# Kernel tuning notes

Measured on AMD Instinct MI355X. Metric: run time of the kernel, lower is better.

Reference implementation:

```python
import jax, jax.numpy as jnp
import numpy as np

G, N, F_IN, H, C = 128, 512, 128, 128, 10
LAMB = 1.0
NEG_SLOPE = 0.2
P_EDGE = 32.0 / N  # avg degree ~32


def setup_inputs() -> dict:
    key = jax.random.key(0)
    ks = jax.random.split(key, 12)
    x = jax.random.normal(ks[0], (G, N, F_IN), dtype=jnp.float32)
    # symmetric 0/1 adjacency without self loops (per-graph dense block)
    a = (jax.random.uniform(ks[1], (G, N, N)) < P_EDGE).astype(jnp.float32)
    adj = jnp.maximum(a, jnp.swapaxes(a, 1, 2)) * (1.0 - jnp.eye(N, dtype=jnp.float32))

    def lin(k, fi, fo):
        return (jax.random.normal(k, (fi, fo), dtype=jnp.float32) / np.float32(np.sqrt(fi)))

    return {
        "x": x, "adj": adj,
        "W1": lin(ks[2], F_IN, H), "b1": jnp.zeros((H,), jnp.float32),
        "W2": lin(ks[3], H, H), "b2": jnp.zeros((H,), jnp.float32),
        "W3": lin(ks[4], H, H), "b3": jnp.zeros((H,), jnp.float32),
        "att1_s": 0.1 * jax.random.normal(ks[5], (H,), dtype=jnp.float32),
        "att1_d": 0.1 * jax.random.normal(ks[6], (H,), dtype=jnp.float32),
        "att2_s": 0.1 * jax.random.normal(ks[7], (H,), dtype=jnp.float32),
        "att2_d": 0.1 * jax.random.normal(ks[8], (H,), dtype=jnp.float32),
        "Wl1": lin(ks[9], 2 * H, H), "bl1": jnp.zeros((H,), jnp.float32),
        "Wl2": lin(ks[10], H, H // 2), "bl2": jnp.zeros((H // 2,), jnp.float32),
        "Wl3": lin(ks[11], H // 2, C), "bl3": jnp.zeros((C,), jnp.float32),
    }


def gcn(x, adj, W, b):
    # GCNConv: D^{-1/2} (A + I) D^{-1/2} X W + b  (self-loop weight 1, edge weights in adj)
    deg = adj.sum(-1) + 1.0                              # [G, n]
    dinv = jax.lax.rsqrt(deg)
    xw = x @ W                                           # [G, n, H]
    agg = jnp.einsum('gij,gjf->gif', adj, dinv[..., None] * xw)
    return dinv[..., None] * agg + (dinv * dinv)[..., None] * xw + b


def info_score(x, adj):
    # HGP-SL node information score: row-wise L1 norm of (I - D^{-1} A) X
    deg = jnp.maximum(adj.sum(-1), 1.0)
    agg = jnp.einsum('gij,gjf->gif', adj, x) / deg[..., None]
    return jnp.sum(jnp.abs(x - agg), axis=-1)            # [G, n]


def hgpsl_pool(x, adj, att_s, att_d, k):
    # top-k node selection by information score, then structure learning:
    # dense (sample=False) path: e_ij = leaky_relu(att.[x_i||x_j]) + lamb*A_ij, softmax over j
    s = info_score(x, adj)
    _, idx = jax.lax.top_k(s, k)                         # [G, k]
    xk = jnp.take_along_axis(x, idx[..., None], axis=1)  # [G, k, H]
    g = jnp.arange(x.shape[0])[:, None, None]
    ak = adj[g, idx[:, :, None], idx[:, None, :]]        # induced adjacency [G, k, k]
    e = jax.nn.leaky_relu((xk @ att_s)[:, :, None] + (xk @ att_d)[:, None, :], NEG_SLOPE)
    attn = jax.nn.softmax(e + LAMB * ak, axis=-1)        # new learned edge weights
    return xk, attn


def readout(x):
    # gmp || gap over nodes
    return jnp.concatenate([x.max(axis=1), x.mean(axis=1)], axis=-1)


def reference(x, adj, W1, b1, W2, b2, W3, b3, att1_s, att1_d, att2_s, att2_d,
              Wl1, bl1, Wl2, bl2, Wl3, bl3):
    h = jax.nn.relu(gcn(x, adj, W1, b1))
    h, a1 = hgpsl_pool(h, adj, att1_s, att1_d, N // 2)
    x1 = readout(h)
    h = jax.nn.relu(gcn(h, a1, W2, b2))
    h, a2 = hgpsl_pool(h, a1, att2_s, att2_d, N // 4)
    x2 = readout(h)
    h = jax.nn.relu(gcn(h, a2, W3, b3))
    x3 = readout(h)
    z = jax.nn.relu(x1) + jax.nn.relu(x2) + jax.nn.relu(x3)
    z = jax.nn.relu(z @ Wl1 + bl1)
    z = jax.nn.relu(z @ Wl2 + bl2)
    return jax.nn.softmax(z @ Wl3 + bl3, axis=-1)
```

## Files before the change

### kernel.cpp

```cpp
#include <hip/hip_runtime.h>

#define Gg   128
#define N1   512
#define FH   128
#define K1   256
#define K2   128

typedef __bf16 bf16x8 __attribute__((ext_vector_type(8)));
typedef float  floatx4 __attribute__((ext_vector_type(4)));

__device__ inline float wredsum(float v) {
#pragma unroll
    for (int o = 32; o; o >>= 1) v += __shfl_xor(v, o, 64);
    return v;
}
__device__ inline float wredmax(float v) {
#pragma unroll
    for (int o = 32; o; o >>= 1) v = fmaxf(v, __shfl_xor(v, o, 64));
    return v;
}
__device__ inline unsigned short bf_rne(float x) {
    unsigned u = __float_as_uint(x);
    return (unsigned short)((u + 0x7fffu + ((u >> 16) & 1u)) >> 16);
}

__global__ __launch_bounds__(256) void k_prep(const float* __restrict__ adj,
        float* __restrict__ dinv_gcn, float* __restrict__ dinv_info) {
    int wave = threadIdx.x >> 6, lane = threadIdx.x & 63;
    long long row = (long long)blockIdx.x * 4 + wave;
    const float* ar = adj + row * N1;
    float s = 0.f;
#pragma unroll
    for (int c = 0; c < 2; ++c) {
        float4 v = *(const float4*)(ar + lane * 8 + c * 4);
        s += (v.x + v.y) + (v.z + v.w);
    }
    s = wredsum(s);
    if (lane == 0) {
        dinv_gcn[row]  = rsqrtf(s + 1.0f);
        dinv_info[row] = 1.0f / fmaxf(s, 1.0f);
    }
}

__global__ __launch_bounds__(256) void k_tsplit(const float* __restrict__ feat,
        unsigned short* __restrict__ Thi, unsigned short* __restrict__ Tmid,
        unsigned short* __restrict__ Tlo) {
    __shared__ float tile[64 * 65];
    int b = blockIdx.x;
    int g = b >> 4, rb = (b >> 1) & 7, cb = b & 1;
    int t = threadIdx.x;
    {
        int r0 = t >> 4, c4 = t & 15;
#pragma unroll
        for (int i = 0; i < 4; ++i) {
            int r = r0 + i * 16;
            float4 v = *(const float4*)(feat + ((long long)g * 512 + rb * 64 + r) * 128 + cb * 64 + c4 * 4);
            tile[r * 65 + c4 * 4 + 0] = v.x;
            tile[r * 65 + c4 * 4 + 1] = v.y;
            tile[r * 65 + c4 * 4 + 2] = v.z;
            tile[r * 65 + c4 * 4 + 3] = v.w;
        }
    }
    __syncthreads();
    int tf = t >> 2, chunk = t & 3;
    unsigned short hbuf[16] __attribute__((aligned(16)));
    unsigned short mbuf[16] __attribute__((aligned(16)));
    unsigned short lbuf[16] __attribute__((aligned(16)));
#pragma unroll
    for (int i = 0; i < 16; ++i) {
        int m = chunk * 16 + i;
        float v = tile[m * 65 + tf];
        unsigned short h = bf_rne(v);
        float fh = __uint_as_float((unsigned)h << 16);
        float r1 = v - fh;
        unsigned short md = bf_rne(r1);
        float fm = __uint_as_float((unsigned)md << 16);
        float r2 = r1 - fm;
        unsigned short lo = bf_rne(r2);
        hbuf[i] = h; mbuf[i] = md; lbuf[i] = lo;
    }
    long long obase = ((long long)g * 128 + cb * 64 + tf) * 512 + rb * 64 + chunk * 16;
    *(uint4*)(Thi + obase)      = *(const uint4*)&hbuf[0];
    *(uint4*)(Thi + obase + 8)  = *(const uint4*)&hbuf[8];
    *(uint4*)(Tmid + obase)     = *(const uint4*)&mbuf[0];
    *(uint4*)(Tmid + obase + 8) = *(const uint4*)&mbuf[8];
    *(uint4*)(Tlo + obase)      = *(const uint4*)&lbuf[0];
    *(uint4*)(Tlo + obase + 8)  = *(const uint4*)&lbuf[8];
}

template<int EPI>
__global__ __launch_bounds__(256) void k_aggmm(const float* __restrict__ adjf,
        const unsigned short* __restrict__ Bhi, const unsigned short* __restrict__ Bmid,
        const unsigned short* __restrict__ Blo,
        const float* __restrict__ dvec, const float* __restrict__ hx,
        const float* __restrict__ bias, float* __restrict__ outH, float* __restrict__ outS) {
    __shared__ unsigned short Al[128 * 40];
    __shared__ unsigned short Bls[3][128 * 40];
    __shared__ float sred[2][128];
    int b = blockIdx.x;
    int g  = (b & 7) + ((b >> 5) << 3);
    int rb = (b >> 3) & 3;
    int tid = threadIdx.x;
    int w = tid >> 6, lane = tid & 63;
    int wm = w >> 1, wn = w & 1;
    int ln = lane & 15, quad = lane >> 4;
    floatx4 acc[4][4];
#pragma unroll
    for (int i = 0; i < 4; ++i)
#pragma unroll
        for (int j = 0; j < 4; ++j) { floatx4 z = {0.f, 0.f, 0.f, 0.f}; acc[i][j] = z; }

    const long long arow0 = ((long long)g * 512 + rb * 128) * 512;
    for (int kk = 0; kk < 512; kk += 32) {
        __syncthreads();
#pragma unroll
        for (int i = 0; i < 4; ++i) {
            int id = tid + i * 256;
            int r = id >> 3, c = id & 7;
            float4 v = *(const float4*)(adjf + arow0 + (long long)r * 512 + kk + c * 4);
            ushort4 u;
            u.x = (unsigned short)(__float_as_uint(v.x) >> 16);
            u.y = (unsigned short)(__float_as_uint(v.y) >> 16);
            u.z = (unsigned short)(__float_as_uint(v.z) >> 16);
            u.w = (unsigned short)(__float_as_uint(v.w) >> 16);
            *(ushort4*)&Al[r * 40 + c * 4] = u;
        }
#pragma unroll
        for (int mB = 0; mB < 3; ++mB) {
            const unsigned short* Bp = (mB == 0) ? Bhi : (mB == 1 ? Bmid : Blo);
#pragma unroll
            for (int i = 0; i < 2; ++i) {
                int id = tid + i * 256;
                int r = id >> 2, c = id & 3;
                uint4 u = *(const uint4*)(Bp + ((long long)g * 128 + r) * 512 + kk + c * 8);
                *(uint4*)&Bls[mB][r * 40 + c * 8] = u;
            }
        }
        __syncthreads();
        bf16x8 af[4];
#pragma unroll
        for (int tm = 0; tm < 4; ++tm)
            af[tm] = *(const bf16x8*)&Al[(wm * 64 + tm * 16 + ln) * 40 + quad * 8];
#pragma unroll
        for (int s = 0; s < 3; ++s) {
#pragma unroll
            for (int tn = 0; tn < 4; ++tn) {
                bf16x8 bfr = *(const bf16x8*)&Bls[s][(wn * 64 + tn * 16 + ln) * 40 + quad * 8];
#pragma unroll
                for (int tm = 0; tm < 4; ++tm)
                    acc[tm][tn] = __builtin_amdgcn_mfma_f32_16x16x32_bf16(af[tm], bfr, acc[tm][tn], 0, 0, 0);
            }
        }
    }
    long long rowbase = (long long)g * 512 + rb * 128;
    if (EPI == 0) {
#pragma unroll
        for (int tm = 0; tm < 4; ++tm)
#pragma unroll
        for (int r = 0; r < 4; ++r) {
            int ml = wm * 64 + tm * 16 + quad * 4 + r;
            long long grow = rowbase + ml;
            float di = dvec[grow];
#pragma unroll
            for (int tn = 0; tn < 4; ++tn) {
                int nc = wn * 64 + tn * 16 + ln;
                float hv = hx[grow * 128 + nc];
                float o = fmaxf(fmaf(di, acc[tm][tn][r] + hv, bias[nc]), 0.f);
                outH[grow * 128 + nc] = o;
            }
        }
    } else {
#pragma unroll
        for (int tm = 0; tm < 4; ++tm)
#pragma unroll
        for (int r = 0; r < 4; ++r) {
            int ml = wm * 64 + tm * 16 + quad * 4 + r;
            long long grow = rowbase + ml;
            float di = dvec[grow];
            float v = 0.f;
#pragma unroll
            for (int tn = 0; tn < 4; ++tn) {
                int nc = wn * 64 + tn * 16 + ln;
                float hv = hx[grow * 128 + nc];
                v += fabsf(hv - acc[tm][tn][r] * di);
            }
            v += __shfl_xor(v, 1); v += __shfl_xor(v, 2);
            v += __shfl_xor(v, 4); v += __shfl_xor(v, 8);
            if (ln == 0) sred[wn][ml] = v;
        }
        __syncthreads();
        if (tid < 128) outS[rowbase + tid] = sred[0][tid] + sred[1][tid];
    }
}

__global__ __launch_bounds__(256) void k_gemm_rw(const float* __restrict__ A,
        const float* __restrict__ W, float* __restrict__ C,
        const float* __restrict__ rs) {
    __shared__ float Al[64][68];
    __shared__ float Wl[64][132];
    long long row0 = (long long)blockIdx.x * 64;
    int tid = threadIdx.x, tr = tid >> 4, tc = tid & 15;
    float acc[4][8] = {};
    for (int ch = 0; ch < 2; ++ch) {
        for (int p = tid; p < 1024; p += 256) {
            int r = p >> 4, c4 = p & 15;
            *(float4*)&Al[r][c4 * 4] = *(const float4*)(A + (row0 + r) * 128 + ch * 64 + c4 * 4);
        }
        for (int p = tid; p < 2048; p += 256) {
            int r = p >> 5, c4 = p & 31;
            *(float4*)&Wl[r][c4 * 4] = *(const float4*)(W + (ch * 64 + r) * 128 + c4 * 4);
        }
        __syncthreads();
        for (int k = 0; k < 64; ++k) {
            float4 w0 = *(const float4*)&Wl[k][tc * 8];
            float4 w1 = *(const float4*)&Wl[k][tc * 8 + 4];
            float w[8] = {w0.x, w0.y, w0.z, w0.w, w1.x, w1.y, w1.z, w1.w};
#pragma unroll
            for (int i = 0; i < 4; ++i) {
                float a = Al[tr * 4 + i][k];
#pragma unroll
                for (int j = 0; j < 8; ++j) acc[i][j] = fmaf(a, w[j], acc[i][j]);
            }
        }
        __syncthreads();
    }
#pragma unroll
    for (int i = 0; i < 4; ++i) {
        long long r = row0 + tr * 4 + i;
        float sc = rs ? rs[r] : 1.0f;
        *(float4*)(C + r * 128 + tc * 8)     = make_float4(sc * acc[i][0], sc * acc[i][1], sc * acc[i][2], sc * acc[i][3]);
        *(float4*)(C + r * 128 + tc * 8 + 4) = make_float4(sc * acc[i][4], sc * acc[i][5], sc * acc[i][6], sc * acc[i][7]);
    }
}

template<int NT, int KSEL>
__global__ __launch_bounds__(256) void k_topk(const float* __restrict__ s, int* __restrict__ idx) {
    __shared__ unsigned long long keys[NT];
    int g = blockIdx.x;
    const float* sg = s + g * NT;
    for (int t = threadIdx.x; t < NT; t += 256) {
        unsigned int b = __float_as_uint(sg[t]);
        unsigned int ord = (b & 0x80000000u) ? ~b : (b | 0x80000000u);
        keys[t] = ((unsigned long long)(~ord) << 32) | (unsigned int)t;
    }
    __syncthreads();
    for (int k = 2; k <= NT; k <<= 1) {
        for (int j = k >> 1; j > 0; j >>= 1) {
            for (int i = threadIdx.x; i < NT; i += 256) {
                int l = i ^ j;
                if (l > i) {
                    bool dir = ((i & k) == 0);
                    unsigned long long a = keys[i], b2 = keys[l];
                    bool sw = dir ? (a > b2) : (a < b2);
                    if (sw) { keys[i] = b2; keys[l] = a; }
                }
            }
            __syncthreads();
        }
    }
    for (int t = threadIdx.x; t < KSEL; t += 256)
        idx[g * KSEL + t] = (int)(keys[t] & 0xffffffffu);
}

template<int KK>
__global__ __launch_bounds__(256) void k_gather(const float* __restrict__ h, int srcN,
        const int* __restrict__ idx, const float* __restrict__ atts, const float* __restrict__ attd,
        float* __restrict__ xk, float* __restrict__ as_, float* __restrict__ ad_) {
    int wave = threadIdx.x >> 6, lane = threadIdx.x & 63;
    int r = blockIdx.x * 4 + wave;
    int g = r / KK;
    int j = idx[r];
    float2 v = *(const float2*)(h + ((long long)g * srcN + j) * 128 + lane * 2);
    *(float2*)(xk + (long long)r * 128 + lane * 2) = v;
    float2 sv = *(const float2*)(atts + lane * 2);
    float2 dv = *(const float2*)(attd + lane * 2);
    float ps = v.x * sv.x + v.y * sv.y;
    float pd = v.x * dv.x + v.y * dv.y;
    ps = wredsum(ps); pd = wredsum(pd);
    if (lane == 0) { as_[r] = ps; ad_[r] = pd; }
}

template<int KK, int SRCN>
__global__ __launch_bounds__(256) void k_attn(const float* __restrict__ adjSrc,
        const int* __restrict__ idx, const float* __restrict__ as_, const float* __restrict__ ad_,
        float* __restrict__ attn, float* __restrict__ dgo, float* __restrict__ dio) {
    constexpr int E = KK / 64;
    __shared__ int   idxL[KK];
    __shared__ float adL[KK];
    __shared__ float rowL[4][SRCN];
    int bpg = KK / 4;
    int g = blockIdx.x / bpg;
    int wave = threadIdx.x >> 6, lane = threadIdx.x & 63;
    int i = (blockIdx.x % bpg) * 4 + wave;
    for (int t = threadIdx.x; t < KK; t += 256) { idxL[t] = idx[g * KK + t]; adL[t] = ad_[g * KK + t]; }
    __syncthreads();
    int ri = idxL[i];
    const float* arow = adjSrc + ((long long)g * SRCN + ri) * SRCN;
    for (int c = lane; c < SRCN; c += 64) rowL[wave][c] = arow[c];
    float asi = as_[g * KK + i];
    float vals[E];
    float m = -1e30f;
#pragma unroll
    for (int e = 0; e < E; ++e) {
        int j = e * 64 + lane;
        float x = asi + adL[j];
        x = (x >= 0.f) ? x : 0.2f * x;
        x += rowL[wave][idxL[j]];
        vals[e] = x; m = fmaxf(m, x);
    }
    m = wredmax(m);
    float S = 0.f;
#pragma unroll
    for (int e = 0; e < E; ++e) { vals[e] = expf(vals[e] - m); S += vals[e]; }
    S = wredsum(S);
    float inv = 1.f / S, rs = 0.f;
    float* orow = attn + ((long long)g * KK + i) * KK;
#pragma unroll
    for (int e = 0; e < E; ++e) { float p = vals[e] * inv; rs += p; orow[e * 64 + lane] = p; }
    rs = wredsum(rs);
    if (lane == 0) { dgo[g * KK + i] = rsqrtf(rs + 1.f); dio[g * KK + i] = 1.f / fmaxf(rs, 1.f); }
}

template<int KK>
__global__ __launch_bounds__(128) void k_readout(const float* __restrict__ xk, float* __restrict__ xo) {
    int g = blockIdx.x, f = threadIdx.x;
    const float* p = xk + (long long)g * KK * 128 + f;
    float m = -1e30f, s = 0.f;
    for (int r = 0; r < KK; ++r) { float v = p[r * 128]; m = fmaxf(m, v); s += v; }
    xo[g * 256 + f] = m;
    xo[g * 256 + 128 + f] = s * (1.0f / KK);
}

template<int KK, bool SCALEY, int EPI>
__global__ __launch_bounds__(256) void k_agg(const float* __restrict__ A, const float* __restrict__ Y,
        const float* __restrict__ dg, const float* __restrict__ di_,
        const float* __restrict__ bias, const float* __restrict__ hx,
        float* __restrict__ outH, float* __restrict__ outS) {
    __shared__ float Al[64][68];
    __shared__ float Yl[64][132];
    __shared__ float red[64][17];
    constexpr int RB = KK / 64;
    int g = blockIdx.x / RB;
    int rb = blockIdx.x % RB;
    const float* Ag = A + (long long)g * KK * KK;
    const float* Yg = Y + (long long)g * KK * 128;
    int tid = threadIdx.x, tr = tid >> 4, tc = tid & 15;
    float acc[4][8] = {};
    for (int ch = 0; ch < KK / 64; ++ch) {
        for (int p = tid; p < 1024; p += 256) {
            int r = p >> 4, c4 = p & 15;
            *(float4*)&Al[r][c4 * 4] = *(const float4*)(Ag + (rb * 64 + r) * KK + ch * 64 + c4 * 4);
        }
        for (int p = tid; p < 2048; p += 256) {
            int r = p >> 5, c4 = p & 31;
            float4 v = *(const float4*)(Yg + (ch * 64 + r) * 128 + c4 * 4);
            if (SCALEY) { float sc = dg[g * KK + ch * 64 + r]; v.x *= sc; v.y *= sc; v.z *= sc; v.w *= sc; }
            *(float4*)&Yl[r][c4 * 4] = v;
        }
        __syncthreads();
        for (int k = 0; k < 64; ++k) {
            float4 w0 = *(const float4*)&Yl[k][tc * 8];
            float4 w1 = *(const float4*)&Yl[k][tc * 8 + 4];
            float w[8] = {w0.x, w0.y, w0.z, w0.w, w1.x, w1.y, w1.z, w1.w};
#pragma unroll
            for (int i = 0; i < 4; ++i) {
                float a = Al[tr * 4 + i][k];
#pragma unroll
                for (int j = 0; j < 8; ++j) acc[i][j] = fmaf(a, w[j], acc[i][j]);
            }
        }
        __syncthreads();
    }
    int i0 = rb * 64 + tr * 4;
    if (EPI == 0) {
#pragma unroll
        for (int i = 0; i < 4; ++i) {
            long long gi = (long long)g * KK + i0 + i;
            float d = dg[gi], dd = d * d;
            float4 x0 = *(const float4*)(hx + gi * 128 + tc * 8);
            float4 x1 = *(const float4*)(hx + gi * 128 + tc * 8 + 4);
            float4 b0 = *(const float4*)(bias + tc * 8);
            float4 b1 = *(const float4*)(bias + tc * 8 + 4);
            float4 o0, o1;
            o0.x = fmaxf(fmaf(d, acc[i][0], fmaf(dd, x0.x, b0.x)), 0.f);
            o0.y = fmaxf(fmaf(d, acc[i][1], fmaf(dd, x0.y, b0.y)), 0.f);
            o0.z = fmaxf(fmaf(d, acc[i][2], fmaf(dd, x0.z, b0.z)), 0.f);
            o0.w = fmaxf(fmaf(d, acc[i][3], fmaf(dd, x0.w, b0.w)), 0.f);
            o1.x = fmaxf(fmaf(d, acc[i][4], fmaf(dd, x1.x, b1.x)), 0.f);
            o1.y = fmaxf(fmaf(d, acc[i][5], fmaf(dd, x1.y, b1.y)), 0.f);
            o1.z = fmaxf(fmaf(d, acc[i][6], fmaf(dd, x1.z, b1.z)), 0.f);
            o1.w = fmaxf(fmaf(d, acc[i][7], fmaf(dd, x1.w, b1.w)), 0.f);
            *(float4*)(outH + gi * 128 + tc * 8)     = o0;
            *(float4*)(outH + gi * 128 + tc * 8 + 4) = o1;
        }
    } else {
#pragma unroll
        for (int i = 0; i < 4; ++i) {
            long long gi = (long long)g * KK + i0 + i;
            float d = di_[gi];
            float4 x0 = *(const float4*)(hx + gi * 128 + tc * 8);
            float4 x1 = *(const float4*)(hx + gi * 128 + tc * 8 + 4);
            float p = fabsf(x0.x - acc[i][0] * d) + fabsf(x0.y - acc[i][1] * d)
                    + fabsf(x0.z - acc[i][2] * d) + fabsf(x0.w - acc[i][3] * d)
                    + fabsf(x1.x - acc[i][4] * d) + fabsf(x1.y - acc[i][5] * d)
                    + fabsf(x1.z - acc[i][6] * d) + fabsf(x1.w - acc[i][7] * d);
            red[tr * 4 + i][tc] = p;
        }
        __syncthreads();
        if (tid < 64) {
            float s = 0.f;
#pragma unroll
            for (int t = 0; t < 16; ++t) s += red[tid][t];
            outS[(long long)g * KK + rb * 64 + tid] = s;
        }
    }
}

__global__ __launch_bounds__(128) void k_mlp(const float* __restrict__ x1, const float* __restrict__ x2,
        const float* __restrict__ x3,
        const float* __restrict__ Wl1, const float* __restrict__ bl1,
        const float* __restrict__ Wl2, const float* __restrict__ bl2,
        const float* __restrict__ Wl3, const float* __restrict__ bl3,
        float* __restrict__ out) {
    __shared__ float z[256], z1[128], z2[64], lg[10];
    int g = blockIdx.x, t = threadIdx.x;
    for (int k = t; k < 256; k += 128)
        z[k] = fmaxf(x1[g * 256 + k], 0.f) + fmaxf(x2[g * 256 + k], 0.f) + fmaxf(x3[g * 256 + k], 0.f);
    __syncthreads();
    {
        float acc = bl1[t];
        for (int k = 0; k < 256; ++k) acc = fmaf(z[k], Wl1[k * 128 + t], acc);
        z1[t] = fmaxf(acc, 0.f);
    }
    __syncthreads();
    if (t < 64) {
        float acc = bl2[t];
        for (int k = 0; k < 128; ++k) acc = fmaf(z1[k], Wl2[k * 64 + t], acc);
        z2[t] = fmaxf(acc, 0.f);
    }
    __syncthreads();
    if (t < 10) {
        float acc = bl3[t];
        for (int k = 0; k < 64; ++k) acc = fmaf(z2[k], Wl3[k * 10 + t], acc);
        lg[t] = acc;
    }
    __syncthreads();
    if (t == 0) {
        float m = -1e30f;
        for (int c = 0; c < 10; ++c) m = fmaxf(m, lg[c]);
        float S = 0.f;
        float e[10];
        for (int c = 0; c < 10; ++c) { e[c] = expf(lg[c] - m); S += e[c]; }
        float inv = 1.f / S;
        for (int c = 0; c < 10; ++c) out[g * 10 + c] = e[c] * inv;
    }
}

extern "C" void kernel_launch(void* const* d_in, const int* in_sizes, int n_in,
                              void* d_out, int out_size, void* d_ws, size_t ws_size,
                              hipStream_t stream) {
    const float* x     = (const float*)d_in[0];
    const float* adj   = (const float*)d_in[1];
    const float* W1    = (const float*)d_in[2];
    const float* b1    = (const float*)d_in[3];
    const float* W2    = (const float*)d_in[4];
    const float* b2    = (const float*)d_in[5];
    const float* W3    = (const float*)d_in[6];
    const float* b3    = (const float*)d_in[7];
    const float* att1s = (const float*)d_in[8];
    const float* att1d = (const float*)d_in[9];
    const float* att2s = (const float*)d_in[10];
    const float* att2d = (const float*)d_in[11];
    const float* Wl1   = (const float*)d_in[12];
    const float* bl1   = (const float*)d_in[13];
    const float* Wl2   = (const float*)d_in[14];
    const float* bl2   = (const float*)d_in[15];
    const float* Wl3   = (const float*)d_in[16];
    const float* bl3   = (const float*)d_in[17];
    float* out = (float*)d_out;

    char* ws = (char*)d_ws;
    unsigned short* Thi  = (unsigned short*)(ws + 0);
    unsigned short* Tmid = (unsigned short*)(ws + 16777216);
    unsigned short* Tlo  = (unsigned short*)(ws + 33554432);
    float* xk1 = (float*)(ws + 0);
    float* xw2 = (float*)(ws + 16777216);
    float* h2  = (float*)(ws + 33554432);
    float* xk2 = (float*)(ws + 16777216);
    float* a2  = (float*)(ws + 25165824);
    float* xw3 = (float*)(ws + 0);
    float* h3  = (float*)(ws + 8388608);
    float* dxw1 = (float*)(ws + 50331648);
    float* h1   = dxw1;
    float* a1   = dxw1;
    float* s1      = (float*)(ws + 83886080);
    int*   idx1    = (int*)  (ws + 84148224);
    float* as1     = (float*)(ws + 84279296);
    float* ad1     = (float*)(ws + 84410368);
    float* dinv_g1 = (float*)(ws + 84541440);
    float* dinv_i1 = (float*)(ws + 84803584);
    float* dinv_g2 = (float*)(ws + 85065728);
    float* dinv_i2 = (float*)(ws + 85196800);
    float* x1r     = (float*)(ws + 85327872);
    float* s2      = (float*)(ws + 85458944);
    int*   idx2    = (int*)  (ws + 85590016);
    float* as2     = (float*)(ws + 85655552);
    float* ad2     = (float*)(ws + 85721088);
    float* dinv_g3 = (float*)(ws + 85786624);
    float* dinv_i3 = (float*)(ws + 85852160);
    float* x2r     = (float*)(ws + 85917696);
    float* x3r     = (float*)(ws + 86048768);

    k_prep<<<Gg * N1 / 4, 256, 0, stream>>>(adj, dinv_g1, dinv_i1);
    k_gemm_rw<<<Gg * N1 / 64, 256, 0, stream>>>(x, W1, dxw1, dinv_g1);
    k_tsplit<<<Gg * 16, 256, 0, stream>>>(dxw1, Thi, Tmid, Tlo);
    k_aggmm<0><<<Gg * 4, 256, 0, stream>>>(adj, Thi, Tmid, Tlo, dinv_g1, dxw1, b1, h1, nullptr);
    k_tsplit<<<Gg * 16, 256, 0, stream>>>(h1, Thi, Tmid, Tlo);
    k_aggmm<1><<<Gg * 4, 256, 0, stream>>>(adj, Thi, Tmid, Tlo, dinv_i1, h1, nullptr, nullptr, s1);
    k_topk<N1, K1><<<Gg, 256, 0, stream>>>(s1, idx1);
    k_gather<K1><<<Gg * K1 / 4, 256, 0, stream>>>(h1, N1, idx1, att1s, att1d, xk1, as1, ad1);
    k_readout<K1><<<Gg, 128, 0, stream>>>(xk1, x1r);
    k_attn<K1, N1><<<Gg * K1 / 4, 256, 0, stream>>>(adj, idx1, as1, ad1, a1, dinv_g2, dinv_i2);

    k_gemm_rw<<<Gg * K1 / 64, 256, 0, stream>>>(xk1, W2, xw2, nullptr);
    k_agg<K1, true, 0><<<Gg * (K1 / 64), 256, 0, stream>>>(a1, xw2, dinv_g2, dinv_i2, b2, xw2, h2, nullptr);
    k_agg<K1, false, 1><<<Gg * (K1 / 64), 256, 0, stream>>>(a1, h2, dinv_g2, dinv_i2, b2, h2, nullptr, s2);
    k_topk<K1, K2><<<Gg, 256, 0, stream>>>(s2, idx2);
    k_gather<K2><<<Gg * K2 / 4, 256, 0, stream>>>(h2, K1, idx2, att2s, att2d, xk2, as2, ad2);
    k_readout<K2><<<Gg, 128, 0, stream>>>(xk2, x2r);
    k_attn<K2, K1><<<Gg * K2 / 4, 256, 0, stream>>>(a1, idx2, as2, ad2, a2, dinv_g3, dinv_i3);

    k_gemm_rw<<<Gg * K2 / 64, 256, 0, stream>>>(xk2, W3, xw3, nullptr);
    k_agg<K2, true, 0><<<Gg * (K2 / 64), 256, 0, stream>>>(a2, xw3, dinv_g3, dinv_i3, b3, xw3, h3, nullptr);
    k_readout<K2><<<Gg, 128, 0, stream>>>(h3, x3r);

    k_mlp<<<Gg, 128, 0, stream>>>(x1r, x2r, x3r, Wl1, bl1, Wl2, bl2, Wl3, bl3, out);
}
```

Baseline: 606.8 us.

## Fuse bf16 splitting into GEMM epilogues and use MFMA for pooled-graph aggregation

The transpose-and-split kernels are removed. The three-way bf16 split is now written directly from the feature GEMM and GCN aggregation epilogues, and k_prep writes a bf16 copy of the adjacency so the aggregation loads half the bytes. The later pooled-level aggregations, which previously used scalar fp32 k_agg, now run on MFMA with 3-way split attention matrices produced by new attn kernels. In exchange the workspace grows a lot, and there is extra split work plus several shared-memory passes in the epilogues.

```diff
diff --git a/kernel.cpp b/kernel.cpp
--- a/kernel.cpp
+++ b/kernel.cpp
@@ -6,6 +6,7 @@
 #define K1   256
 #define K2   128
 
+typedef unsigned short ush;
 typedef __bf16 bf16x8 __attribute__((ext_vector_type(8)));
 typedef float  floatx4 __attribute__((ext_vector_type(4)));
 
@@ -19,22 +20,37 @@
     for (int o = 32; o; o >>= 1) v = fmaxf(v, __shfl_xor(v, o, 64));
     return v;
 }
-__device__ inline unsigned short bf_rne(float x) {
+__device__ inline ush bf_rne(float x) {
     unsigned u = __float_as_uint(x);
-    return (unsigned short)((u + 0x7fffu + ((u >> 16) & 1u)) >> 16);
+    return (ush)((u + 0x7fffu + ((u >> 16) & 1u)) >> 16);
+}
+__device__ inline float bf2f(ush u) { return __uint_as_float((unsigned)u << 16); }
+__device__ inline void split3(float v, ush& h, ush& m, ush& l) {
+    h = bf_rne(v);
+    float r1 = v - bf2f(h);
+    m = bf_rne(r1);
+    l = bf_rne(r1 - bf2f(m));
 }
 
 __global__ __launch_bounds__(256) void k_prep(const float* __restrict__ adj,
-        float* __restrict__ dinv_gcn, float* __restrict__ dinv_info) {
+        float* __restrict__ dinv_gcn, float* __restrict__ dinv_info,
+        ush* __restrict__ adjbf) {
     int wave = threadIdx.x >> 6, lane = threadIdx.x & 63;
     long long row = (long long)blockIdx.x * 4 + wave;
     const float* ar = adj + row * N1;
+    ush* br = adjbf + row * N1;
     float s = 0.f;
+    ush ub[8] __attribute__((aligned(16)));
 #pragma unroll
     for (int c = 0; c < 2; ++c) {
         float4 v = *(const float4*)(ar + lane * 8 + c * 4);
         s += (v.x + v.y) + (v.z + v.w);
-    }
+        ub[c * 4 + 0] = (ush)(__float_as_uint(v.x) >> 16);
+        ub[c * 4 + 1] = (ush)(__float_as_uint(v.y) >> 16);
+        ub[c * 4 + 2] = (ush)(__float_as_uint(v.z) >> 16);
+        ub[c * 4 + 3] = (ush)(__float_as_uint(v.w) >> 16);
+    }
+    *(uint4*)(br + lane * 8) = *(const uint4*)&ub[0];
     s = wredsum(s);
     if (lane == 0) {
         dinv_gcn[row]  = rsqrtf(s + 1.0f);
@@ -42,61 +58,80 @@
     }
 }
 
-__global__ __launch_bounds__(256) void k_tsplit(const float* __restrict__ feat,
-        unsigned short* __restrict__ Thi, unsigned short* __restrict__ Tmid,
-        unsigned short* __restrict__ Tlo) {
-    __shared__ float tile[64 * 65];
-    int b = blockIdx.x;
-    int g = b >> 4, rb = (b >> 1) & 7, cb = b & 1;
-    int t = threadIdx.x;
-    {
-        int r0 = t >> 4, c4 = t & 15;
-#pragma unroll
-        for (int i = 0; i < 4; ++i) {
-            int r = r0 + i * 16;
-            float4 v = *(const float4*)(feat + ((long long)g * 512 + rb * 64 + r) * 128 + cb * 64 + c4 * 4);
-            tile[r * 65 + c4 * 4 + 0] = v.x;
-            tile[r * 65 + c4 * 4 + 1] = v.y;
-            tile[r * 65 + c4 * 4 + 2] = v.z;
-            tile[r * 65 + c4 * 4 + 3] = v.w;
-        }
-    }
-    __syncthreads();
-    int tf = t >> 2, chunk = t & 3;
-    unsigned short hbuf[16] __attribute__((aligned(16)));
-    unsigned short mbuf[16] __attribute__((aligned(16)));
-    unsigned short lbuf[16] __attribute__((aligned(16)));
-#pragma unroll
-    for (int i = 0; i < 16; ++i) {
-        int m = chunk * 16 + i;
-        float v = tile[m * 65 + tf];
-        unsigned short h = bf_rne(v);
-        float fh = __uint_as_float((unsigned)h << 16);
-        float r1 = v - fh;
-        unsigned short md = bf_rne(r1);
-        float fm = __uint_as_float((unsigned)md << 16);
-        float r2 = r1 - fm;
-        unsigned short lo = bf_rne(r2);
-        hbuf[i] = h; mbuf[i] = md; lbuf[i] = lo;
-    }
-    long long obase = ((long long)g * 128 + cb * 64 + tf) * 512 + rb * 64 + chunk * 16;
-    *(uint4*)(Thi + obase)      = *(const uint4*)&hbuf[0];
-    *(uint4*)(Thi + obase + 8)  = *(const uint4*)&hbuf[8];
-    *(uint4*)(Tmid + obase)     = *(const uint4*)&mbuf[0];
-    *(uint4*)(Tmid + obase + 8) = *(const uint4*)&mbuf[8];
-    *(uint4*)(Tlo + obase)      = *(const uint4*)&lbuf[0];
-    *(uint4*)(Tlo + obase + 8)  = *(const uint4*)&lbuf[8];
-}
-
-template<int EPI>
-__global__ __launch_bounds__(256) void k_aggmm(const float* __restrict__ adjf,
-        const unsigned short* __restrict__ Bhi, const unsigned short* __restrict__ Bmid,
-        const unsigned short* __restrict__ Blo,
+template<int KD>
+__global__ __launch_bounds__(256) void k_gemm_rwt(const float* __restrict__ A,
+        const float* __restrict__ W, float* __restrict__ C,
+        const float* __restrict__ rs,
+        ush* __restrict__ Thi, ush* __restrict__ Tmid, ush* __restrict__ Tlo) {
+    __shared__ float Al[64 * 68];
+    __shared__ float Wl[64 * 132];
+    long long row0 = (long long)blockIdx.x * 64;
+    int tid = threadIdx.x, tr = tid >> 4, tc = tid & 15;
+    float acc[4][8] = {};
+    for (int ch = 0; ch < 2; ++ch) {
+        for (int p = tid; p < 1024; p += 256) {
+            int r = p >> 4, c4 = p & 15;
+            *(float4*)&Al[r * 68 + c4 * 4] = *(const float4*)(A + (row0 + r) * 128 + ch * 64 + c4 * 4);
+        }
+        for (int p = tid; p < 2048; p += 256) {
+            int r = p >> 5, c4 = p & 31;
+            *(float4*)&Wl[r * 132 + c4 * 4] = *(const float4*)(W + (ch * 64 + r) * 128 + c4 * 4);
+        }
+        __syncthreads();
+        for (int k = 0; k < 64; ++k) {
+            float4 w0 = *(const float4*)&Wl[k * 132 + tc * 8];
+            float4 w1 = *(const float4*)&Wl[k * 132 + tc * 8 + 4];
+            float w[8] = {w0.x, w0.y, w0.z, w0.w, w1.x, w1.y, w1.z, w1.w};
+#pragma unroll
+            for (int i = 0; i < 4; ++i) {
+                float a = Al[(tr * 4 + i) * 68 + k];
+#pragma unroll
+                for (int j = 0; j < 8; ++j) acc[i][j] = fmaf(a, w[j], acc[i][j]);
+            }
+        }
+        __syncthreads();
+    }
+    float* Cl = Wl;
+#pragma unroll
+    for (int i = 0; i < 4; ++i) {
+        long long r = row0 + tr * 4 + i;
+        float sc = rs ? rs[r] : 1.0f;
+        float v[8];
+#pragma unroll
+        for (int j = 0; j < 8; ++j) v[j] = sc * acc[i][j];
+        *(float4*)(C + r * 128 + tc * 8)     = make_float4(v[0], v[1], v[2], v[3]);
+        *(float4*)(C + r * 128 + tc * 8 + 4) = make_float4(v[4], v[5], v[6], v[7]);
+#pragma unroll
+        for (int j = 0; j < 8; ++j) Cl[(tr * 4 + i) * 129 + tc * 8 + j] = v[j];
+    }
+    __syncthreads();
+    int f = tid >> 1, half = tid & 1;
+    int g = (int)(row0 / KD), rk0 = (int)(row0 % KD);
+    ush hb[32] __attribute__((aligned(16)));
+    ush mb[32] __attribute__((aligned(16)));
+    ush lb[32] __attribute__((aligned(16)));
+#pragma unroll
+    for (int i = 0; i < 32; ++i)
+        split3(Cl[(half * 32 + i) * 129 + f], hb[i], mb[i], lb[i]);
+    long long ob = ((long long)g * 128 + f) * KD + rk0 + half * 32;
+#pragma unroll
+    for (int q = 0; q < 4; ++q) {
+        *(uint4*)(Thi  + ob + q * 8) = *(const uint4*)&hb[q * 8];
+        *(uint4*)(Tmid + ob + q * 8) = *(const uint4*)&mb[q * 8];
+        *(uint4*)(Tlo  + ob + q * 8) = *(const uint4*)&lb[q * 8];
+    }
+}
+
+template<int EPI, bool WRT>
+__global__ __launch_bounds__(256) void k_aggmm2(const ush* __restrict__ adjbf,
+        const ush* __restrict__ Bhi, const ush* __restrict__ Bmid, const ush* __restrict__ Blo,
         const float* __restrict__ dvec, const float* __restrict__ hx,
-        const float* __restrict__ bias, float* __restrict__ outH, float* __restrict__ outS) {
-    __shared__ unsigned short Al[128 * 40];
-    __shared__ unsigned short Bls[3][128 * 40];
-    __shared__ float sred[2][128];
+        const float* __restrict__ bias, float* __restrict__ outH, float* __restrict__ outS,
+        ush* __restrict__ Thi, ush* __restrict__ Tmid, ush* __restrict__ Tlo) {
+    __shared__ char smem[41984] __attribute__((aligned(16)));
+    ush* Asm = (ush*)smem;
+    float* sred = (float*)(smem + 40960);
+    float* Cl = (float*)smem;
     int b = blockIdx.x;
     int g  = (b & 7) + ((b >> 5) << 3);
     int rb = (b >> 3) & 3;
@@ -110,42 +145,38 @@
 #pragma unroll
         for (int j = 0; j < 4; ++j) { floatx4 z = {0.f, 0.f, 0.f, 0.f}; acc[i][j] = z; }
 
-    const long long arow0 = ((long long)g * 512 + rb * 128) * 512;
+    const long long abase = ((long long)g * 512 + rb * 128) * 512;
+    const long long bbase = (long long)g * 128 * 512;
     for (int kk = 0; kk < 512; kk += 32) {
         __syncthreads();
 #pragma unroll
-        for (int i = 0; i < 4; ++i) {
+        for (int i = 0; i < 2; ++i) {
             int id = tid + i * 256;
-            int r = id >> 3, c = id & 7;
-            float4 v = *(const float4*)(adjf + arow0 + (long long)r * 512 + kk + c * 4);
-            ushort4 u;
-            u.x = (unsigned short)(__float_as_uint(v.x) >> 16);
-            u.y = (unsigned short)(__float_as_uint(v.y) >> 16);
-            u.z = (unsigned short)(__float_as_uint(v.z) >> 16);
-            u.w = (unsigned short)(__float_as_uint(v.w) >> 16);
-            *(ushort4*)&Al[r * 40 + c * 4] = u;
+            int r = id >> 2, c = id & 3;
+            *(uint4*)&Asm[r * 40 + c * 8] = *(const uint4*)(adjbf + abase + (long long)r * 512 + kk + c * 8);
         }
 #pragma unroll
         for (int mB = 0; mB < 3; ++mB) {
-            const unsigned short* Bp = (mB == 0) ? Bhi : (mB == 1 ? Bmid : Blo);
+            const ush* Bp = (mB == 0) ? Bhi : (mB == 1 ? Bmid : Blo);
+            ush* dst = (ush*)(smem + 10240 + mB * 10240);
 #pragma unroll
             for (int i = 0; i < 2; ++i) {
                 int id = tid + i * 256;
                 int r = id >> 2, c = id & 3;
-                uint4 u = *(const uint4*)(Bp + ((long long)g * 128 + r) * 512 + kk + c * 8);
-                *(uint4*)&Bls[mB][r * 40 + c * 8] = u;
+                *(uint4*)&dst[r * 40 + c * 8] = *(const uint4*)(Bp + bbase + (long long)r * 512 + kk + c * 8);
             }
         }
         __syncthreads();
         bf16x8 af[4];
 #pragma unroll
         for (int tm = 0; tm < 4; ++tm)
-            af[tm] = *(const bf16x8*)&Al[(wm * 64 + tm * 16 + ln) * 40 + quad * 8];
+            af[tm] = *(const bf16x8*)&Asm[(wm * 64 + tm * 16 + ln) * 40 + quad * 8];
 #pragma unroll
         for (int s = 0; s < 3; ++s) {
+            const ush* Bs = (const ush*)(smem + 10240 + s * 10240);
 #pragma unroll
             for (int tn = 0; tn < 4; ++tn) {
-                bf16x8 bfr = *(const bf16x8*)&Bls[s][(wn * 64 + tn * 16 + ln) * 40 + quad * 8];
+                bf16x8 bfr = *(const bf16x8*)&Bs[(wn * 64 + tn * 16 + ln) * 40 + quad * 8];
 #pragma unroll
                 for (int tm = 0; tm < 4; ++tm)
                     acc[tm][tn] = __builtin_amdgcn_mfma_f32_16x16x32_bf16(af[tm], bfr, acc[tm][tn], 0, 0, 0);
@@ -158,15 +189,44 @@
         for (int tm = 0; tm < 4; ++tm)
 #pragma unroll
         for (int r = 0; r < 4; ++r) {
-            int ml = wm * 64 + tm * 16 + quad * 4 + r;
-            long long grow = rowbase + ml;
+            long long grow = rowbase + wm * 64 + tm * 16 + quad * 4 + r;
             float di = dvec[grow];
 #pragma unroll
             for (int tn = 0; tn < 4; ++tn) {
                 int nc = wn * 64 + tn * 16 + ln;
-                float hv = hx[grow * 128 + nc];
-                float o = fmaxf(fmaf(di, acc[tm][tn][r] + hv, bias[nc]), 0.f);
+                float o = fmaxf(fmaf(di, acc[tm][tn][r] + hx[grow * 128 + nc], bias[nc]), 0.f);
                 outH[grow * 128 + nc] = o;
+                acc[tm][tn][r] = o;
+            }
+        }
+        if (WRT) {
+#pragma unroll
+            for (int p = 0; p < 2; ++p) {
+                __syncthreads();
+                if (wm == p) {
+#pragma unroll
+                    for (int tm = 0; tm < 4; ++tm)
+#pragma unroll
+                    for (int r = 0; r < 4; ++r)
+#pragma unroll
+                    for (int tn = 0; tn < 4; ++tn)
+                        Cl[(tm * 16 + quad * 4 + r) * 129 + wn * 64 + tn * 16 + ln] = acc[tm][tn][r];
+                }
+                __syncthreads();
+                int f = tid >> 1, half = tid & 1;
+                ush hb[32] __attribute__((aligned(16)));
+                ush mb[32] __attribute__((aligned(16)));
+                ush lb[32] __attribute__((aligned(16)));
+#pragma unroll
+                for (int i = 0; i < 32; ++i)
+                    split3(Cl[(half * 32 + i) * 129 + f], hb[i], mb[i], lb[i]);
+                long long ob = ((long long)g * 128 + f) * 512 + rb * 128 + p * 64 + half * 32;
+#pragma unroll
+                for (int q = 0; q < 4; ++q) {
+                    *(uint4*)(Thi  + ob + q * 8) = *(const uint4*)&hb[q * 8];
+                    *(uint4*)(Tmid + ob + q * 8) = *(const uint4*)&mb[q * 8];
+                    *(uint4*)(Tlo  + ob + q * 8) = *(const uint4*)&lb[q * 8];
+                }
             }
         }
     } else {
@@ -181,55 +241,151 @@
 #pragma unroll
             for (int tn = 0; tn < 4; ++tn) {
                 int nc = wn * 64 + tn * 16 + ln;
-                float hv = hx[grow * 128 + nc];
-                v += fabsf(hv - acc[tm][tn][r] * di);
+                v += fabsf(hx[grow * 128 + nc] - acc[tm][tn][r] * di);
             }
             v += __shfl_xor(v, 1); v += __shfl_xor(v, 2);
             v += __shfl_xor(v, 4); v += __shfl_xor(v, 8);
-            if (ln == 0) sred[wn][ml] = v;
-        }
-        __syncthreads();
-        if (tid < 128) outS[rowbase + tid] = sred[0][tid] + sred[1][tid];
-    }
-}
-
-__global__ __launch_bounds__(256) void k_gemm_rw(const float* __restrict__ A,
-        const float* __restrict__ W, float* __restrict__ C,
-        const float* __restrict__ rs) {
-    __shared__ float Al[64][68];
-    __shared__ float Wl[64][132];
-    long long row0 = (long long)blockIdx.x * 64;
-    int tid = threadIdx.x, tr = tid >> 4, tc = tid & 15;
-    float acc[4][8] = {};
-    for (int ch = 0; ch < 2; ++ch) {
-        for (int p = tid; p < 1024; p += 256) {
-            int r = p >> 4, c4 = p & 15;
-            *(float4*)&Al[r][c4 * 4] = *(const float4*)(A + (row0 + r) * 128 + ch * 64 + c4 * 4);
-        }
-        for (int p = tid; p < 2048; p += 256) {
-            int r = p >> 5, c4 = p & 31;
-            *(float4*)&Wl[r][c4 * 4] = *(const float4*)(W + (ch * 64 + r) * 128 + c4 * 4);
-        }
-        __syncthreads();
-        for (int k = 0; k < 64; ++k) {
-            float4 w0 = *(const float4*)&Wl[k][tc * 8];
-            float4 w1 = *(const float4*)&Wl[k][tc * 8 + 4];
-            float w[8] = {w0.x, w0.y, w0.z, w0.w, w1.x, w1.y, w1.z, w1.w};
-#pragma unroll
-            for (int i = 0; i < 4; ++i) {
-                float a = Al[tr * 4 + i][k];
-#pragma unroll
-                for (int j = 0; j < 8; ++j) acc[i][j] = fmaf(a, w[j], acc[i][j]);
-            }
-        }
-        __syncthreads();
-    }
-#pragma unroll
-    for (int i = 0; i < 4; ++i) {
-        long long r = row0 + tr * 4 + i;
-        float sc = rs ? rs[r] : 1.0f;
-        *(float4*)(C + r * 128 + tc * 8)     = make_float4(sc * acc[i][0], sc * acc[i][1], sc * acc[i][2], sc * acc[i][3]);
-        *(float4*)(C + r * 128 + tc * 8 + 4) = make_float4(sc * acc[i][4], sc * acc[i][5], sc * acc[i][6], sc * acc[i][7]);
+            if (ln == 0) sred[wn * 128 + ml] = v;
+        }
+        __syncthreads();
+        if (tid < 128) outS[rowbase + tid] = sred[tid] + sred[128 + tid];
+    }
+}
+
+template<int KD, int EPI, bool WRT>
+__global__ __launch_bounds__(256) void k_aggp(
+        const ush* __restrict__ Ahi, const ush* __restrict__ Amid, const ush* __restrict__ Alo,
+        const ush* __restrict__ Yhi, const ush* __restrict__ Ymid, const ush* __restrict__ Ylo,
+        const float* __restrict__ dvec, const float* __restrict__ hx,
+        const float* __restrict__ bias, float* __restrict__ outH, float* __restrict__ outS,
+        ush* __restrict__ Thi, ush* __restrict__ Tmid, ush* __restrict__ Tlo) {
+    __shared__ char smem[62464] __attribute__((aligned(16)));
+    float* sred = (float*)(smem + 61440);
+    float* Cl = (float*)smem;
+    int b = blockIdx.x;
+    int g, rb;
+    if (KD == 256) { g = (b & 7) + ((b >> 4) << 3); rb = (b >> 3) & 1; }
+    else           { g = b; rb = 0; }
+    int tid = threadIdx.x;
+    int w = tid >> 6, lane = tid & 63;
+    int wm = w >> 1, wn = w & 1;
+    int ln = lane & 15, quad = lane >> 4;
+    floatx4 acc[4][4];
+#pragma unroll
+    for (int i = 0; i < 4; ++i)
+#pragma unroll
+        for (int j = 0; j < 4; ++j) { floatx4 z = {0.f, 0.f, 0.f, 0.f}; acc[i][j] = z; }
+
+    const long long abase = ((long long)g * KD + rb * 128) * KD;
+    const long long ybase = (long long)g * 128 * KD;
+    for (int kk = 0; kk < KD; kk += 32) {
+        __syncthreads();
+#pragma unroll
+        for (int mP = 0; mP < 3; ++mP) {
+            const ush* Ap = (mP == 0) ? Ahi : (mP == 1 ? Amid : Alo);
+            const ush* Yp = (mP == 0) ? Yhi : (mP == 1 ? Ymid : Ylo);
+            ush* dstA = (ush*)(smem + mP * 10240);
+            ush* dstB = (ush*)(smem + 30720 + mP * 10240);
+#pragma unroll
+            for (int i = 0; i < 2; ++i) {
+                int id = tid + i * 256;
+                int r = id >> 2, c = id & 3;
+                *(uint4*)&dstA[r * 40 + c * 8] = *(const uint4*)(Ap + abase + (long long)r * KD + kk + c * 8);
+                *(uint4*)&dstB[r * 40 + c * 8] = *(const uint4*)(Yp + ybase + (long long)r * KD + kk + c * 8);
+            }
+        }
+        __syncthreads();
+        bf16x8 af[3][4];
+#pragma unroll
+        for (int mP = 0; mP < 3; ++mP) {
+            const ush* As = (const ush*)(smem + mP * 10240);
+#pragma unroll
+            for (int tm = 0; tm < 4; ++tm)
+                af[mP][tm] = *(const bf16x8*)&As[(wm * 64 + tm * 16 + ln) * 40 + quad * 8];
+        }
+#pragma unroll
+        for (int tn = 0; tn < 4; ++tn) {
+            int brow = (wn * 64 + tn * 16 + ln) * 40 + quad * 8;
+            bf16x8 bh = *(const bf16x8*)&((const ush*)(smem + 30720))[brow];
+            bf16x8 bm = *(const bf16x8*)&((const ush*)(smem + 40960))[brow];
+            bf16x8 bl = *(const bf16x8*)&((const ush*)(smem + 51200))[brow];
+#pragma unroll
+            for (int tm = 0; tm < 4; ++tm) {
+                acc[tm][tn] = __builtin_amdgcn_mfma_f32_16x16x32_bf16(af[0][tm], bh, acc[tm][tn], 0, 0, 0);
+                acc[tm][tn] = __builtin_amdgcn_mfma_f32_16x16x32_bf16(af[0][tm], bm, acc[tm][tn], 0, 0, 0);
+                acc[tm][tn] = __builtin_amdgcn_mfma_f32_16x16x32_bf16(af[1][tm], bh, acc[tm][tn], 0, 0, 0);
+                acc[tm][tn] = __builtin_amdgcn_mfma_f32_16x16x32_bf16(af[0][tm], bl, acc[tm][tn], 0, 0, 0);
+                acc[tm][tn] = __builtin_amdgcn_mfma_f32_16x16x32_bf16(af[1][tm], bm, acc[tm][tn], 0, 0, 0);
+                acc[tm][tn] = __builtin_amdgcn_mfma_f32_16x16x32_bf16(af[2][tm], bh, acc[tm][tn], 0, 0, 0);
+            }
+        }
+    }
+    long long rowbase = (long long)g * KD + rb * 128;
+    if (EPI == 0) {
+#pragma unroll
+        for (int tm = 0; tm < 4; ++tm)
+#pragma unroll
+        for (int r = 0; r < 4; ++r) {
+            long long grow = rowbase + wm * 64 + tm * 16 + quad * 4 + r;
+            float di = dvec[grow];
+#pragma unroll
+            for (int tn = 0; tn < 4; ++tn) {
+                int nc = wn * 64 + tn * 16 + ln;
+                float o = fmaxf(fmaf(di, acc[tm][tn][r] + hx[grow * 128 + nc], bias[nc]), 0.f);
+                outH[grow * 128 + nc] = o;
+                acc[tm][tn][r] = o;
+            }
+        }
+        if (WRT) {
+#pragma unroll
+            for (int p = 0; p < 2; ++p) {
+                __syncthreads();
+                if (wm == p) {
+#pragma unroll
+                    for (int tm = 0; tm < 4; ++tm)
+#pragma unroll
+                    for (int r = 0; r < 4; ++r)
+#pragma unroll
+                    for (int tn = 0; tn < 4; ++tn)
+                        Cl[(tm * 16 + quad * 4 + r) * 129 + wn * 64 + tn * 16 + ln] = acc[tm][tn][r];
+                }
+                __syncthreads();
+                int f = tid >> 1, half = tid & 1;
+                ush hb[32] __attribute__((aligned(16)));
+                ush mb[32] __attribute__((aligned(16)));
+                ush lb[32] __attribute__((aligned(16)));
+#pragma unroll
+                for (int i = 0; i < 32; ++i)
+                    split3(Cl[(half * 32 + i) * 129 + f], hb[i], mb[i], lb[i]);
+                long long ob = ((long long)g * 128 + f) * KD + rb * 128 + p * 64 + half * 32;
+#pragma unroll
+                for (int q = 0; q < 4; ++q) {
+                    *(uint4*)(Thi  + ob + q * 8) = *(const uint4*)&hb[q * 8];
+                    *(uint4*)(Tmid + ob + q * 8) = *(const uint4*)&mb[q * 8];
+                    *(uint4*)(Tlo  + ob + q * 8) = *(const uint4*)&lb[q * 8];
+                }
+            }
+        }
+    } else {
+#pragma unroll
+        for (int tm = 0; tm < 4; ++tm)
+#pragma unroll
+        for (int r = 0; r < 4; ++r) {
+            int ml = wm * 64 + tm * 16 + quad * 4 + r;
+            long long grow = rowbase + ml;
+            float di = dvec[grow];
+            float v = 0.f;
+#pragma unroll
+            for (int tn = 0; tn < 4; ++tn) {
+                int nc = wn * 64 + tn * 16 + ln;
+                v += fabsf(hx[grow * 128 + nc] - acc[tm][tn][r] * di);
+            }
+            v += __shfl_xor(v, 1); v += __shfl_xor(v, 2);
+            v += __shfl_xor(v, 4); v += __shfl_xor(v, 8);
+            if (ln == 0) sred[wn * 128 + ml] = v;
+        }
+        __syncthreads();
+        if (tid < 128) outS[rowbase + tid] = sred[tid] + sred[128 + tid];
     }
 }
 
@@ -280,28 +436,26 @@
     if (lane == 0) { as_[r] = ps; ad_[r] = pd; }
 }
 
-template<int KK, int SRCN>
-__global__ __launch_bounds__(256) void k_attn(const float* __restrict__ adjSrc,
+__global__ __launch_bounds__(256) void k_attn1(const ush* __restrict__ adjbf,
         const int* __restrict__ idx, const float* __restrict__ as_, const float* __restrict__ ad_,
-        float* __restrict__ attn, float* __restrict__ dgo, float* __restrict__ dio) {
-    constexpr int E = KK / 64;
-    __shared__ int   idxL[KK];
-    __shared__ float adL[KK];
-    __shared__ float rowL[4][SRCN];
-    int bpg = KK / 4;
-    int g = blockIdx.x / bpg;
+        float* __restrict__ a1, ush* __restrict__ Ahi, ush* __restrict__ Amid, ush* __restrict__ Alo,
+        float* __restrict__ dgo, float* __restrict__ dio) {
+    __shared__ int   idxL[K1];
+    __shared__ float adL[K1];
+    __shared__ float rowL[4][N1];
+    int g = blockIdx.x / (K1 / 4);
     int wave = threadIdx.x >> 6, lane = threadIdx.x & 63;
-    int i = (blockIdx.x % bpg) * 4 + wave;
-    for (int t = threadIdx.x; t < KK; t += 256) { idxL[t] = idx[g * KK + t]; adL[t] = ad_[g * KK + t]; }
+    int i = (blockIdx.x % (K1 / 4)) * 4 + wave;
+    for (int t = threadIdx.x; t < K1; t += 256) { idxL[t] = idx[g * K1 + t]; adL[t] = ad_[g * K1 + t]; }
     __syncthreads();
     int ri = idxL[i];
-    const float* arow = adjSrc + ((long long)g * SRCN + ri) * SRCN;
-    for (int c = lane; c < SRCN; c += 64) rowL[wave][c] = arow[c];
-    float asi = as_[g * KK + i];
-    float vals[E];
+    const ush* arow = adjbf + ((long long)g * N1 + ri) * N1;
+    for (int c = lane; c < N1; c += 64) rowL[wave][c] = bf2f(arow[c]);
+    float asi = as_[g * K1 + i];
+    float vals[4];
     float m = -1e30f;
 #pragma unroll
-    for (int e = 0; e < E; ++e) {
+    for (int e = 0; e < 4; ++e) {
         int j = e * 64 + lane;
         float x = asi + adL[j];
         x = (x >= 0.f) ? x : 0.2f * x;
@@ -311,108 +465,88 @@
     m = wredmax(m);
     float S = 0.f;
 #pragma unroll
-    for (int e = 0; e < E; ++e) { vals[e] = expf(vals[e] - m); S += vals[e]; }
+    for (int e = 0; e < 4; ++e) { vals[e] = expf(vals[e] - m); S += vals[e]; }
     S = wredsum(S);
     float inv = 1.f / S, rs = 0.f;
-    float* orow = attn + ((long long)g * KK + i) * KK;
-#pragma unroll
-    for (int e = 0; e < E; ++e) { float p = vals[e] * inv; rs += p; orow[e * 64 + lane] = p; }
+    float* orow = a1 + ((long long)g * K1 + i) * K1;
+#pragma unroll
+    for (int e = 0; e < 4; ++e) {
+        float p = vals[e] * inv; rs += p;
+        orow[e * 64 + lane] = p;
+        rowL[wave][e * 64 + lane] = p;
+    }
     rs = wredsum(rs);
-    if (lane == 0) { dgo[g * KK + i] = rsqrtf(rs + 1.f); dio[g * KK + i] = 1.f / fmaxf(rs, 1.f); }
+    if (lane == 0) { dgo[g * K1 + i] = rsqrtf(rs + 1.f); dio[g * K1 + i] = 1.f / fmaxf(rs, 1.f); }
+    long long sb = ((long long)g * K1 + i) * K1 + lane * 4;
+    ush hb[4], mb[4], lb[4];
+#pragma unroll
+    for (int q = 0; q < 4; ++q) split3(rowL[wave][lane * 4 + q], hb[q], mb[q], lb[q]);
+    *(ushort4*)(Ahi  + sb) = make_ushort4(hb[0], hb[1], hb[2], hb[3]);
+    *(ushort4*)(Amid + sb) = make_ushort4(mb[0], mb[1], mb[2], mb[3]);
+    *(ushort4*)(Alo  + sb) = make_ushort4(lb[0], lb[1], lb[2], lb[3]);
+}
+
+__global__ __launch_bounds__(256) void k_attn2(const float* __restrict__ a1,
+        const int* __restrict__ idx, const float* __restrict__ as_, const float* __restrict__ ad_,
+        ush* __restrict__ Ahi, ush* __restrict__ Amid, ush* __restrict__ Alo,
+        float* __restrict__ dgo) {
+    __shared__ int   idxL[K2];
+    __shared__ float adL[K2];
+    __shared__ float rowL[4][K1];
+    int g = blockIdx.x / (K2 / 4);
+    int wave = threadIdx.x >> 6, lane = threadIdx.x & 63;
+    int i = (blockIdx.x % (K2 / 4)) * 4 + wave;
+    for (int t = threadIdx.x; t < K2; t += 256) { idxL[t] = idx[g * K2 + t]; adL[t] = ad_[g * K2 + t]; }
+    __syncthreads();
+    int ri = idxL[i];
+    const float* arow = a1 + ((long long)g * K1 + ri) * K1;
+    for (int c = lane; c < K1; c += 64) rowL[wave][c] = arow[c];
+    float asi = as_[g * K2 + i];
+    float vals[2];
+    float m = -1e30f;
+#pragma unroll
+    for (int e = 0; e < 2; ++e) {
+        int j = e * 64 + lane;
+        float x = asi + adL[j];
+        x = (x >= 0.f) ? x : 0.2f * x;
+        x += rowL[wave][idxL[j]];
+        vals[e] = x; m = fmaxf(m, x);
+    }
+    m = wredmax(m);
+    float S = 0.f;
+#pragma unroll
+    for (int e = 0; e < 2; ++e) { vals[e] = expf(vals[e] - m); S += vals[e]; }
+    S = wredsum(S);
+    float inv = 1.f / S, rs = 0.f;
+#pragma unroll
+    for (int e = 0; e < 2; ++e) {
+        float p = vals[e] * inv; rs += p;
+        rowL[wave][e * 64 + lane] = p;
+    }
+    rs = wredsum(rs);
+    if (lane == 0) dgo[g * K2 + i] = rsqrtf(rs + 1.f);
+    long long sb = ((long long)g * K2 + i) * K2 + lane * 2;
+    ush hb[2], mb[2], lb[2];
+#pragma unroll
+    for (int q = 0; q < 2; ++q) split3(rowL[wave][lane * 2 + q], hb[q], mb[q], lb[q]);
+    *(ushort2*)(Ahi  + sb) = make_ushort2(hb[0], hb[1]);
+    *(ushort2*)(Amid + sb) = make_ushort2(mb[0], mb[1]);
+    *(ushort2*)(Alo  + sb) = make_ushort2(lb[0], lb[1]);
 }
 
 template<int KK>
-__global__ __launch_bounds__(128) void k_readout(const float* __restrict__ xk, float* __restrict__ xo) {
-    int g = blockIdx.x, f = threadIdx.x;
-    const float* p = xk + (long long)g * KK * 128 + f;
+__global__ __launch_bounds__(256) void k_readout(const float* __restrict__ xk, float* __restrict__ xo) {
+    __shared__ float sm[2][128], ss[2][128];
+    int g = blockIdx.x, t = threadIdx.x;
+    int f = t & 127, half = t >> 7;
+    const float* p = xk + ((long long)g * KK + half * (KK / 2)) * 128 + f;
     float m = -1e30f, s = 0.f;
-    for (int r = 0; r < KK; ++r) { float v = p[r * 128]; m = fmaxf(m, v); s += v; }
-    xo[g * 256 + f] = m;
-    xo[g * 256 + 128 + f] = s * (1.0f / KK);
-}
-
-template<int KK, bool SCALEY, int EPI>
-__global__ __launch_bounds__(256) void k_agg(const float* __restrict__ A, const float* __restrict__ Y,
-        const float* __restrict__ dg, const float* __restrict__ di_,
-        const float* __restrict__ bias, const float* __restrict__ hx,
-        float* __restrict__ outH, float* __restrict__ outS) {
-    __shared__ float Al[64][68];
-    __shared__ float Yl[64][132];
-    __shared__ float red[64][17];
-    constexpr int RB = KK / 64;
-    int g = blockIdx.x / RB;
-    int rb = blockIdx.x % RB;
-    const float* Ag = A + (long long)g * KK * KK;
-    const float* Yg = Y + (long long)g * KK * 128;
-    int tid = threadIdx.x, tr = tid >> 4, tc = tid & 15;
-    float acc[4][8] = {};
-    for (int ch = 0; ch < KK / 64; ++ch) {
-        for (int p = tid; p < 1024; p += 256) {
-            int r = p >> 4, c4 = p & 15;
-            *(float4*)&Al[r][c4 * 4] = *(const float4*)(Ag + (rb * 64 + r) * KK + ch * 64 + c4 * 4);
-        }
-        for (int p = tid; p < 2048; p += 256) {
-            int r = p >> 5, c4 = p & 31;
-            float4 v = *(const float4*)(Yg + (ch * 64 + r) * 128 + c4 * 4);
-            if (SCALEY) { float sc = dg[g * KK + ch * 64 + r]; v.x *= sc; v.y *= sc; v.z *= sc; v.w *= sc; }
-            *(float4*)&Yl[r][c4 * 4] = v;
-        }
-        __syncthreads();
-        for (int k = 0; k < 64; ++k) {
-            float4 w0 = *(const float4*)&Yl[k][tc * 8];
-            float4 w1 = *(const float4*)&Yl[k][tc * 8 + 4];
-            float w[8] = {w0.x, w0.y, w0.z, w0.w, w1.x, w1.y, w1.z, w1.w};
-#pragma unroll
-            for (int i = 0; i < 4; ++i) {
-                float a = Al[tr * 4 + i][k];
-#pragma unroll
-                for (int j = 0; j < 8; ++j) acc[i][j] = fmaf(a, w[j], acc[i][j]);
-            }
-        }
-        __syncthreads();
-    }
-    int i0 = rb * 64 + tr * 4;
-    if (EPI == 0) {
-#pragma unroll
-        for (int i = 0; i < 4; ++i) {
-            long long gi = (long long)g * KK + i0 + i;
-            float d = dg[gi], dd = d * d;
-            float4 x0 = *(const float4*)(hx + gi * 128 + tc * 8);
-            float4 x1 = *(const float4*)(hx + gi * 128 + tc * 8 + 4);
-            float4 b0 = *(const float4*)(bias + tc * 8);
-            float4 b1 = *(const float4*)(bias + tc * 8 + 4);
-            float4 o0, o1;
-            o0.x = fmaxf(fmaf(d, acc[i][0], fmaf(dd, x0.x, b0.x)), 0.f);
-            o0.y = fmaxf(fmaf(d, acc[i][1], fmaf(dd, x0.y, b0.y)), 0.f);
-            o0.z = fmaxf(fmaf(d, acc[i][2], fmaf(dd, x0.z, b0.z)), 0.f);
-            o0.w = fmaxf(fmaf(d, acc[i][3], fmaf(dd, x0.w, b0.w)), 0.f);
-            o1.x = fmaxf(fmaf(d, acc[i][4], fmaf(dd, x1.x, b1.x)), 0.f);
-            o1.y = fmaxf(fmaf(d, acc[i][5], fmaf(dd, x1.y, b1.y)), 0.f);
-            o1.z = fmaxf(fmaf(d, acc[i][6], fmaf(dd, x1.z, b1.z)), 0.f);
-            o1.w = fmaxf(fmaf(d, acc[i][7], fmaf(dd, x1.w, b1.w)), 0.f);
-            *(float4*)(outH + gi * 128 + tc * 8)     = o0;
-            *(float4*)(outH + gi * 128 + tc * 8 + 4) = o1;
-        }
-    } else {
-#pragma unroll
-        for (int i = 0; i < 4; ++i) {
-            long long gi = (long long)g * KK + i0 + i;
-            float d = di_[gi];
-            float4 x0 = *(const float4*)(hx + gi * 128 + tc * 8);
-            float4 x1 = *(const float4*)(hx + gi * 128 + tc * 8 + 4);
-            float p = fabsf(x0.x - acc[i][0] * d) + fabsf(x0.y - acc[i][1] * d)
-                    + fabsf(x0.z - acc[i][2] * d) + fabsf(x0.w - acc[i][3] * d)
-                    + fabsf(x1.x - acc[i][4] * d) + fabsf(x1.y - acc[i][5] * d)
-                    + fabsf(x1.z - acc[i][6] * d) + fabsf(x1.w - acc[i][7] * d);
-            red[tr * 4 + i][tc] = p;
-        }
-        __syncthreads();
-        if (tid < 64) {
-            float s = 0.f;
-#pragma unroll
-            for (int t = 0; t < 16; ++t) s += red[tid][t];
-            outS[(long long)g * KK + rb * 64 + tid] = s;
-        }
+    for (int r = 0; r < KK / 2; ++r) { float v = p[r * 128]; m = fmaxf(m, v); s += v; }
+    sm[half][f] = m; ss[half][f] = s;
+    __syncthreads();
+    if (t < 128) {
+        xo[g * 256 + t] = fmaxf(sm[0][t], sm[1][t]);
+        xo[g * 256 + 128 + t] = (ss[0][t] + ss[1][t]) * (1.0f / KK);
     }
 }
 
@@ -480,59 +614,82 @@
     float* out = (float*)d_out;
 
     char* ws = (char*)d_ws;
-    unsigned short* Thi  = (unsigned short*)(ws + 0);
-    unsigned short* Tmid = (unsigned short*)(ws + 16777216);
-    unsigned short* Tlo  = (unsigned short*)(ws + 33554432);
-    float* xk1 = (float*)(ws + 0);
-    float* xw2 = (float*)(ws + 16777216);
-    float* h2  = (float*)(ws + 33554432);
-    float* xk2 = (float*)(ws + 16777216);
-    float* a2  = (float*)(ws + 25165824);
-    float* xw3 = (float*)(ws + 0);
-    float* h3  = (float*)(ws + 8388608);
-    float* dxw1 = (float*)(ws + 50331648);
-    float* h1   = dxw1;
-    float* a1   = dxw1;
-    float* s1      = (float*)(ws + 83886080);
-    int*   idx1    = (int*)  (ws + 84148224);
-    float* as1     = (float*)(ws + 84279296);
-    float* ad1     = (float*)(ws + 84410368);
-    float* dinv_g1 = (float*)(ws + 84541440);
-    float* dinv_i1 = (float*)(ws + 84803584);
-    float* dinv_g2 = (float*)(ws + 85065728);
-    float* dinv_i2 = (float*)(ws + 85196800);
-    float* x1r     = (float*)(ws + 85327872);
-    float* s2      = (float*)(ws + 85458944);
-    int*   idx2    = (int*)  (ws + 85590016);
-    float* as2     = (float*)(ws + 85655552);
-    float* ad2     = (float*)(ws + 85721088);
-    float* dinv_g3 = (float*)(ws + 85786624);
-    float* dinv_i3 = (float*)(ws + 85852160);
-    float* x2r     = (float*)(ws + 85917696);
-    float* x3r     = (float*)(ws + 86048768);
-
-    k_prep<<<Gg * N1 / 4, 256, 0, stream>>>(adj, dinv_g1, dinv_i1);
-    k_gemm_rw<<<Gg * N1 / 64, 256, 0, stream>>>(x, W1, dxw1, dinv_g1);
-    k_tsplit<<<Gg * 16, 256, 0, stream>>>(dxw1, Thi, Tmid, Tlo);
-    k_aggmm<0><<<Gg * 4, 256, 0, stream>>>(adj, Thi, Tmid, Tlo, dinv_g1, dxw1, b1, h1, nullptr);
-    k_tsplit<<<Gg * 16, 256, 0, stream>>>(h1, Thi, Tmid, Tlo);
-    k_aggmm<1><<<Gg * 4, 256, 0, stream>>>(adj, Thi, Tmid, Tlo, dinv_i1, h1, nullptr, nullptr, s1);
+    ush*   adjbf  = (ush*)  (ws + 0);
+    ush*   T1hi   = (ush*)  (ws + 67108864);
+    ush*   T1mid  = (ush*)  (ws + 83886080);
+    ush*   T1lo   = (ush*)  (ws + 100663296);
+    ush*   T2hi   = (ush*)  (ws + 117440512);
+    ush*   T2mid  = (ush*)  (ws + 134217728);
+    ush*   T2lo   = (ush*)  (ws + 150994944);
+    float* dxw1   = (float*)(ws + 167772160);
+    float* h1     = dxw1;
+    float* a1     = (float*)(ws + 201326592);
+    ush*   A1hi   = (ush*)  (ws + 234881024);
+    ush*   A1mid  = (ush*)  (ws + 251658240);
+    ush*   A1lo   = (ush*)  (ws + 268435456);
+    ush*   Y2hi   = (ush*)  (ws + 285212672);
+    ush*   Y2mid  = (ush*)  (ws + 293601280);
+    ush*   Y2lo   = (ush*)  (ws + 301989888);
+    ush*   H2hi   = (ush*)  (ws + 310378496);
+    ush*   H2mid  = (ush*)  (ws + 318767104);
+    ush*   H2lo   = (ush*)  (ws + 327155712);
+    float* dxw2   = (float*)(ws + 335544320);
+    float* h2     = (float*)(ws + 352321536);
+    float* xk1    = (float*)(ws + 369098752);
+    float* xk2    = (float*)(ws + 385875968);
+    ush*   A2hi   = (ush*)  (ws + 394264576);
+    ush*   A2mid  = (ush*)  (ws + 398458880);
+    ush*   A2lo   = (ush*)  (ws + 402653184);
+    ush*   Y3hi   = (ush*)  (ws + 406847488);
+    ush*   Y3mid  = (ush*)  (ws + 411041792);
+    ush*   Y3lo   = (ush*)  (ws + 415236096);
+    float* dxw3   = (float*)(ws + 419430400);
+    float* h3     = (float*)(ws + 427819008);
+    float* s1     = (float*)(ws + 436207616);
+    int*   idx1   = (int*)  (ws + 436469760);
+    float* as1    = (float*)(ws + 436600832);
+    float* ad1    = (float*)(ws + 436731904);
+    float* dinv_g1= (float*)(ws + 436862976);
+    float* dinv_i1= (float*)(ws + 437125120);
+    float* dinv_g2= (float*)(ws + 437387264);
+    float* dinv_i2= (float*)(ws + 437518336);
+    float* x1r    = (float*)(ws + 437649408);
+    float* s2     = (float*)(ws + 437780480);
+    int*   idx2   = (int*)  (ws + 437911552);
+    float* as2    = (float*)(ws + 437977088);
+    float* ad2    = (float*)(ws + 438042624);
+    float* dinv_g3= (float*)(ws + 438108160);
+    float* x2r    = (float*)(ws + 438173696);
+    float* x3r    = (float*)(ws + 438304768);
+
+    k_prep<<<Gg * N1 / 4, 256, 0, stream>>>(adj, dinv_g1, dinv_i1, adjbf);
+    k_gemm_rwt<N1><<<Gg * N1 / 64, 256, 0, stream>>>(x, W1, dxw1, dinv_g1, T1hi, T1mid, T1lo);
+    k_aggmm2<0, true><<<Gg * 4, 256, 0, stream>>>(adjbf, T1hi, T1mid, T1lo, dinv_g1, dxw1, b1,
+                                                  h1, nullptr, T2hi, T2mid, T2lo);
+    k_aggmm2<1, false><<<Gg * 4, 256, 0, stream>>>(adjbf, T2hi, T2mid, T2lo, dinv_i1, h1, nullptr,
+                                                   nullptr, s1, nullptr, nullptr, nullptr);
     k_topk<N1, K1><<<Gg, 256, 0, stream>>>(s1, idx1);
     k_gather<K1><<<Gg * K1 / 4, 256, 0, stream>>>(h1, N1, idx1, att1s, att1d, xk1, as1, ad1);
-    k_readout<K1><<<Gg, 128, 0, stream>>>(xk1, x1r);
-    k_attn<K1, N1><<<Gg * K1 / 4, 256, 0, stream>>>(adj, idx1, as1, ad1, a1, dinv_g2, dinv_i2);
-
-    k_gemm_rw<<<Gg * K1 / 64, 256, 0, stream>>>(xk1, W2, xw2, nullptr);
-    k_agg<K1, true, 0><<<Gg * (K1 / 64), 256, 0, stream>>>(a1, xw2, dinv_g2, dinv_i2, b2, xw2, h2, nullptr);
-    k_agg<K1, false, 1><<<Gg * (K1 / 64), 256, 0, stream>>>(a1, h2, dinv_g2, dinv_i2, b2, h2, nullptr, s2);
+    k_readout<K1><<<Gg, 256, 0, stream>>>(xk1, x1r);
+    k_attn1<<<Gg * K1 / 4, 256, 0, stream>>>(adjbf, idx1, as1, ad1, a1, A1hi, A1mid, A1lo,
+                                             dinv_g2, dinv_i2);
+
+    k_gemm_rwt<K1><<<Gg * K1 / 64, 256, 0, stream>>>(xk1, W2, dxw2, dinv_g2, Y2hi, Y2mid, Y2lo);
+    k_aggp<K1, 0, true><<<Gg * 2, 256, 0, stream>>>(A1hi, A1mid, A1lo, Y2hi, Y2mid, Y2lo,
+                                                    dinv_g2, dxw2, b2, h2, nullptr, H2hi, H2mid, H2lo);
+    k_aggp<K1, 1, false><<<Gg * 2, 256, 0, stream>>>(A1hi, A1mid, A1lo, H2hi, H2mid, H2lo,
+                                                     dinv_i2, h2, nullptr, nullptr, s2,
+                                                     nullptr, nullptr, nullptr);
     k_topk<K1, K2><<<Gg, 256, 0, stream>>>(s2, idx2);
     k_gather<K2><<<Gg * K2 / 4, 256, 0, stream>>>(h2, K1, idx2, att2s, att2d, xk2, as2, ad2);
-    k_readout<K2><<<Gg, 128, 0, stream>>>(xk2, x2r);
-    k_attn<K2, K1><<<Gg * K2 / 4, 256, 0, stream>>>(a1, idx2, as2, ad2, a2, dinv_g3, dinv_i3);
-
-    k_gemm_rw<<<Gg * K2 / 64, 256, 0, stream>>>(xk2, W3, xw3, nullptr);
-    k_agg<K2, true, 0><<<Gg * (K2 / 64), 256, 0, stream>>>(a2, xw3, dinv_g3, dinv_i3, b3, xw3, h3, nullptr);
-    k_readout<K2><<<Gg, 128, 0, stream>>>(h3, x3r);
+    k_readout<K2><<<Gg, 256, 0, stream>>>(xk2, x2r);
+    k_attn2<<<Gg * K2 / 4, 256, 0, stream>>>(a1, idx2, as2, ad2, A2hi, A2mid, A2lo, dinv_g3);
+
+    k_gemm_rwt<K2><<<Gg * K2 / 64, 256, 0, stream>>>(xk2, W3, dxw3, dinv_g3, Y3hi, Y3mid, Y3lo);
+    k_aggp<K2, 0, false><<<Gg, 256, 0, stream>>>(A2hi, A2mid, A2lo, Y3hi, Y3mid, Y3lo,
+                                                 dinv_g3, dxw3, b3, h3, nullptr,
+                                                 nullptr, nullptr, nullptr);
+    k_readout<K2><<<Gg, 256, 0, stream>>>(h3, x3r);
 
     k_mlp<<<Gg, 128, 0, stream>>>(x1r, x2r, x3r, Wl1, bl1, Wl2, bl2, Wl3, bl3, out);
 }
```

Measured after the change: 705.0 us. +16.2%, slower.
